# Optimization experiments

Hardware: AMD Instinct MI355X
Metric: run time of the kernel (lower is better)

The kernel has to match this reference:

```python
import jax, jax.numpy as jnp
import numpy as np

EPS = 1e-5  # BatchNorm2d default eps


def _bn(x, gamma, beta, mean, var):
    # inference-mode BN over channel dim (NCHW)
    inv = gamma / jnp.sqrt(var + EPS)
    return x * inv[None, :, None, None] + (beta - mean * inv)[None, :, None, None]


def _shift(x):
    # 4 channel groups shifted by 1 pixel in 4 directions, zero-fill at borders
    C = x.shape[1]
    gc = C // 4
    g0, g1, g2, g3 = (x[:, i * gc:(i + 1) * gc] for i in range(4))
    g0 = jnp.pad(g0[:, :, :, :-1], ((0, 0), (0, 0), (0, 0), (1, 0)))  # shift right (W)
    g1 = jnp.pad(g1[:, :, 1:, :], ((0, 0), (0, 0), (0, 1), (0, 0)))   # shift up (H)
    g2 = jnp.pad(g2[:, :, :, 1:], ((0, 0), (0, 0), (0, 0), (0, 1)))   # shift left (W)
    g3 = jnp.pad(g3[:, :, :-1, :], ((0, 0), (0, 0), (1, 0), (0, 0)))  # shift down (H)
    return jnp.concatenate([g0, g1, g2, g3], axis=1)


def setup_inputs() -> dict:
    key = jax.random.key(0)
    ks = jax.random.split(key, 8)
    B, C1, C2, H, W = 16, 128, 256, 128, 128
    x = jax.random.normal(ks[0], (B, C1, H, W), dtype=jnp.float32)
    w_conv = jax.random.normal(ks[1], (C2, C1, 3, 3), dtype=jnp.float32) * (1.0 / np.sqrt(C1 * 9))
    w_1x1 = jax.random.normal(ks[2], (C2, C2, 1, 1), dtype=jnp.float32) * (1.0 / np.sqrt(C2))
    b_1x1 = jax.random.normal(ks[3], (C2,), dtype=jnp.float32) * 0.05
    gamma = jax.random.uniform(ks[4], (C2,), dtype=jnp.float32, minval=0.5, maxval=1.5)
    beta = jax.random.normal(ks[5], (C2,), dtype=jnp.float32) * 0.1
    bn_mean = jax.random.normal(ks[6], (C2,), dtype=jnp.float32) * 0.1
    bn_var = jax.random.uniform(ks[7], (C2,), dtype=jnp.float32, minval=0.5, maxval=1.5)
    return {"x": x, "w_conv": w_conv, "w_1x1": w_1x1, "b_1x1": b_1x1,
            "gamma": gamma, "beta": beta, "bn_mean": bn_mean, "bn_var": bn_var}


def reference(x, w_conv, w_1x1, b_1x1, gamma, beta, bn_mean, bn_var):
    # conv3x3 (stride 1, 'same' via autopad=1, no bias) + BN + SiLU
    y = jax.lax.conv_general_dilated(
        x, w_conv, window_strides=(1, 1), padding=((1, 1), (1, 1)),
        dimension_numbers=("NCHW", "OIHW", "NCHW"))
    y = jax.nn.silu(_bn(y, gamma, beta, bn_mean, bn_var))
    identity = y
    # shift + conv1x1 (with bias) + same BN + residual + SiLU
    z = _shift(y)
    z = jax.lax.conv_general_dilated(
        z, w_1x1, window_strides=(1, 1), padding=((0, 0), (0, 0)),
        dimension_numbers=("NCHW", "OIHW", "NCHW")) + b_1x1[None, :, None, None]
    z = _bn(z, gamma, beta, bn_mean, bn_var) + identity
    return jax.nn.silu(z)
```

## Files before the change

kernel.cpp:

```cpp
#include <hip/hip_runtime.h>

typedef unsigned short u16;
typedef unsigned int   u32;
typedef __bf16 bf16x8 __attribute__((ext_vector_type(8)));
typedef float  f32x4  __attribute__((ext_vector_type(4)));

__device__ __forceinline__ float bf2f(u16 v){ u32 u = ((u32)v) << 16; float f; __builtin_memcpy(&f,&u,4); return f; }
__device__ __forceinline__ u16 f2bf(float f){ u32 u; __builtin_memcpy(&u,&f,4); u32 r = (u + 0x7FFFu + ((u>>16)&1u)) >> 16; return (u16)r; }
__device__ __forceinline__ float silu(float v){ return v / (1.f + __expf(-v)); }

__device__ __forceinline__ void gload_lds16(const u16* g, u16* l){
  __builtin_amdgcn_global_load_lds((const __attribute__((address_space(1))) void*)g,
                                   (__attribute__((address_space(3))) void*)l, 16, 0, 0);
}

#define FENCE asm volatile("" ::: "memory")
#define BARRIER do{ FENCE; __builtin_amdgcn_s_barrier(); FENCE; }while(0)

#define HP 130
#define XPIX 128
#define YPIX 256
#define XIMG (HP*HP*XPIX)
#define YIMG (HP*HP*YPIX)

__global__ void prep_coef(const float* __restrict__ gamma, const float* __restrict__ beta,
                          const float* __restrict__ mean,  const float* __restrict__ var,
                          const float* __restrict__ b1, float2* __restrict__ coefA, float2* __restrict__ coefB){
  int c = threadIdx.x;
  float s = gamma[c] * rsqrtf(var[c] + 1e-5f);
  float t = beta[c] - mean[c] * s;
  coefA[c] = make_float2(s, t);
  coefB[c] = make_float2(s, b1[c] * s + t);
}

__global__ void repack_w3(const float* __restrict__ w, u16* __restrict__ w3p){
  int idx = blockIdx.x*256 + threadIdx.x;
  int n = idx / 1152, k = idx % 1152;
  int tap = k >> 7, c = k & 127;
  int kh = tap / 3, kw = tap % 3;
  w3p[idx] = f2bf(w[((n*128 + c)*3 + kh)*3 + kw]);
}

__global__ void repack_w1(const float* __restrict__ w, u16* __restrict__ w1p){
  int idx = blockIdx.x*256 + threadIdx.x;
  w1p[idx] = f2bf(w[idx]);
}

__device__ __forceinline__ void halo_pix(int pi, int& hp, int& wp){
  if (pi < 130){ hp = 0; wp = pi; }
  else if (pi < 260){ hp = 129; wp = pi - 130; }
  else { int j = pi - 260; hp = 1 + (j >> 1); wp = (j & 1) ? 129 : 0; }
}
__global__ void zero_halos(u16* __restrict__ xpad, u16* __restrict__ ypad, int cimg){
  int idx = blockIdx.x*256 + threadIdx.x;
  const int NX = cimg*516*16;
  uint4 z = make_uint4(0u,0u,0u,0u);
  if (idx < NX){
    int b = idx / (516*16), rr = idx % (516*16);
    int pi = rr >> 4, cch = rr & 15, hp, wp;
    halo_pix(pi, hp, wp);
    *(uint4*)(xpad + (((size_t)b*HP + hp)*HP + wp)*XPIX + cch*8) = z;
  } else {
    idx -= NX;
    if (idx < cimg*516*32){
      int b = idx / (516*32), rr = idx % (516*32);
      int pi = rr >> 5, cch = rr & 31, hp, wp;
      halo_pix(pi, hp, wp);
      *(uint4*)(ypad + (((size_t)b*HP + hp)*HP + wp)*YPIX + cch*8) = z;
    }
  }
}

__global__ __launch_bounds__(256) void transpose_x(const float* __restrict__ x, u16* __restrict__ xpad, int b0){
  __shared__ u16 s[64][66];
  const int tid = threadIdx.x, bid = blockIdx.x;
  const int ct = bid & 1, wt = (bid >> 1) & 1, row = bid >> 2;
  const int bl = row >> 7, h = row & 127;
  const int c0 = ct << 6, w0 = wt << 6;
  {
    const int lw = tid & 63, lc4 = tid >> 6;
    const size_t xb = ((size_t)(b0 + bl)*128)*16384 + (size_t)h*128 + w0 + lw;
    #pragma unroll
    for (int r = 0; r < 16; ++r){
      int c = r*4 + lc4;
      s[c][lw] = f2bf(x[xb + (size_t)(c0 + c)*16384]);
    }
  }
  __syncthreads();
  {
    const int lw = tid >> 5, lcp = (tid & 31) << 1;
    const size_t pb = ((size_t)bl*HP + h + 1)*HP;
    #pragma unroll
    for (int r = 0; r < 8; ++r){
      int w = r*8 + lw;
      u32 v = (u32)s[lcp][w] | ((u32)s[lcp+1][w] << 16);
      *(u32*)(xpad + (pb + (w0 + w + 1))*XPIX + c0 + lcp) = v;
    }
  }
}


struct StgDesc { const u16* g[2][2]; int l[2][2]; };

__device__ __forceinline__ int offA_of(int Ts){
  int tap = Ts >> 1;
  int kh = (tap*11) >> 5;
  int kw = tap - kh*3;
  return kh*(HP*XPIX) + kw*XPIX + ((Ts & 1) << 6);
}

template<int V>
__device__ __forceinline__ void stage2(u16* lds, const StgDesc& d, int offE){
  gload_lds16(d.g[V][0] + offE, lds + d.l[V][0]);
  gload_lds16(d.g[V][1] + offE, lds + d.l[V][1]);
}

__global__ __launch_bounds__(512, 2) void convA(const u16* __restrict__ xpad, const u16* __restrict__ w3p,
                                                const float2* __restrict__ coefA, u16* __restrict__ ypad){
  __shared__ u16 sA[2][256*64];
  __shared__ u16 sB[2][256*64];
  const int t = threadIdx.x;
  const int nwg = gridDim.x;
  const int bid = blockIdx.x;
  const int bsz = (bid & 7)*(nwg >> 3) + (bid >> 3);
  const int bl = bsz >> 6;
  const int h0 = (bsz & 63) << 1;
  const int lane = t & 63, wave = t >> 6;
  const int wm = wave & 1, wn = wave >> 1;
  const int quad = lane >> 4, l16 = lane & 15;
  const int lc = t & 7;
  const u16* ximg = xpad + (size_t)bl * XIMG;

  StgDesc da, db;
  #pragma unroll
  for (int ho = 0; ho < 2; ++ho)
    #pragma unroll
    for (int q = 0; q < 2; ++q){
      int r = ((t >> 6) << 4) + (q << 3) + ((t >> 3) & 7);
      int p = (ho << 6) + r + (r & 64);
      da.g[ho][q] = ximg + (size_t)((h0 + (p >> 7))*HP + (p & 127))*XPIX + ((lc ^ (p & 7)) << 3);
      da.l[ho][q] = p*64 + lc*8;
    }
  #pragma unroll
  for (int bo = 0; bo < 2; ++bo)
    #pragma unroll
    for (int q = 0; q < 2; ++q){
      int r = ((t >> 6) << 4) + (q << 3) + ((t >> 3) & 7);
      int n = ((r >> 5) << 6) + (bo << 5) + (r & 31);
      db.g[bo][q] = w3p + (size_t)n*1152 + ((lc ^ (n & 7)) << 3);
      db.l[bo][q] = n*64 + lc*8;
    }

  u32 fA[4][2][2], fB[2][2][2];
  #pragma unroll
  for (int i = 0; i < 4; ++i)
    #pragma unroll
    for (int hf = 0; hf < 2; ++hf)
      #pragma unroll
      for (int c = 0; c < 2; ++c){
        int row = wm*128 + hf*64 + i*16 + l16;
        fA[i][hf][c] = row*64 + (((c*4 + quad) ^ (row & 7)) << 3);
      }
  #pragma unroll
  for (int j = 0; j < 2; ++j)
    #pragma unroll
    for (int hf = 0; hf < 2; ++hf)
      #pragma unroll
      for (int c = 0; c < 2; ++c){
        int row = wn*64 + hf*32 + j*16 + l16;
        fB[j][hf][c] = row*64 + (((c*4 + quad) ^ (row & 7)) << 3);
      }

  f32x4 acc[8][4];
  #pragma unroll
  for (int i = 0; i < 8; ++i)
    #pragma unroll
    for (int j = 0; j < 4; ++j){ f32x4 z = {0.f,0.f,0.f,0.f}; acc[i][j] = z; }

  {
    const int o0 = offA_of(0), o1 = offA_of(1);
    stage2<0>(sA[0], da, o0);
    stage2<0>(sB[0], db, 0);
    stage2<1>(sB[0], db, 0);
    stage2<1>(sA[0], da, o0);
    stage2<0>(sA[1], da, o1);
    stage2<0>(sB[1], db, 64);
    stage2<1>(sB[1], db, 64);
    asm volatile("s_waitcnt vmcnt(6)" ::: "memory");
  }
  BARRIER;

  for (int T = 0; T < 18; ++T){
    const int pr = T & 1;
    const u16* A = sA[pr];
    const u16* B = sB[pr];
    u16* An = sA[pr ^ 1];
    bf16x8 a[4][2], b0[2][2], b1[2][2];

    #pragma unroll
    for (int i = 0; i < 4; ++i){
      a[i][0] = *(const bf16x8*)(A + fA[i][0][0]);
      a[i][1] = *(const bf16x8*)(A + fA[i][0][1]);
    }
    #pragma unroll
    for (int j = 0; j < 2; ++j){
      b0[j][0] = *(const bf16x8*)(B + fB[j][0][0]);
      b0[j][1] = *(const bf16x8*)(B + fB[j][0][1]);
    }
    if (T + 1 < 18) stage2<1>(An, da, offA_of(T+1));
    BARRIER;
    __builtin_amdgcn_s_setprio(1);
    #pragma unroll
    for (int i = 0; i < 4; ++i)
      #pragma unroll
      for (int j = 0; j < 2; ++j){
        acc[i][j] = __builtin_amdgcn_mfma_f32_16x16x32_bf16(a[i][0], b0[j][0], acc[i][j], 0, 0, 0);
        acc[i][j] = __builtin_amdgcn_mfma_f32_16x16x32_bf16(a[i][1], b0[j][1], acc[i][j], 0, 0, 0);
      }
    __builtin_amdgcn_s_setprio(0);
    BARRIER;

    #pragma unroll
    for (int j = 0; j < 2; ++j){
      b1[j][0] = *(const bf16x8*)(B + fB[j][1][0]);
      b1[j][1] = *(const bf16x8*)(B + fB[j][1][1]);
    }
    if (T + 2 < 18) stage2<0>((u16*)A, da, offA_of(T+2));
    BARRIER;
    __builtin_amdgcn_s_setprio(1);
    #pragma unroll
    for (int i = 0; i < 4; ++i)
      #pragma unroll
      for (int j = 0; j < 2; ++j){
        acc[i][2+j] = __builtin_amdgcn_mfma_f32_16x16x32_bf16(a[i][0], b1[j][0], acc[i][2+j], 0, 0, 0);
        acc[i][2+j] = __builtin_amdgcn_mfma_f32_16x16x32_bf16(a[i][1], b1[j][1], acc[i][2+j], 0, 0, 0);
      }
    __builtin_amdgcn_s_setprio(0);
    BARRIER;

    #pragma unroll
    for (int i = 0; i < 4; ++i){
      a[i][0] = *(const bf16x8*)(A + fA[i][1][0]);
      a[i][1] = *(const bf16x8*)(A + fA[i][1][1]);
    }
    if (T + 2 < 18) stage2<0>((u16*)(B), db, (T+2)*64);
    BARRIER;
    __builtin_amdgcn_s_setprio(1);
    #pragma unroll
    for (int i = 0; i < 4; ++i)
      #pragma unroll
      for (int j = 0; j < 2; ++j){
        acc[4+i][2+j] = __builtin_amdgcn_mfma_f32_16x16x32_bf16(a[i][0], b1[j][0], acc[4+i][2+j], 0, 0, 0);
        acc[4+i][2+j] = __builtin_amdgcn_mfma_f32_16x16x32_bf16(a[i][1], b1[j][1], acc[4+i][2+j], 0, 0, 0);
      }
    __builtin_amdgcn_s_setprio(0);
    BARRIER;

    if (T + 2 < 18) stage2<1>((u16*)(B), db, (T+2)*64);
    BARRIER;
    __builtin_amdgcn_s_setprio(1);
    #pragma unroll
    for (int i = 0; i < 4; ++i)
      #pragma unroll
      for (int j = 0; j < 2; ++j){
        acc[4+i][j] = __builtin_amdgcn_mfma_f32_16x16x32_bf16(a[i][0], b0[j][0], acc[4+i][j], 0, 0, 0);
        acc[4+i][j] = __builtin_amdgcn_mfma_f32_16x16x32_bf16(a[i][1], b0[j][1], acc[4+i][j], 0, 0, 0);
      }
    __builtin_amdgcn_s_setprio(0);
    if (T < 16)       asm volatile("s_waitcnt vmcnt(6)" ::: "memory");
    else if (T == 16) asm volatile("s_waitcnt vmcnt(0)" ::: "memory");
    BARRIER;
  }

  float2 co[4];
  #pragma unroll
  for (int j = 0; j < 4; ++j) co[j] = coefA[wn*64 + j*16 + l16];
  #pragma unroll
  for (int ig = 0; ig < 8; ++ig){
    const int pb = wm*128 + ig*16 + quad*4;
    #pragma unroll
    for (int r = 0; r < 4; ++r){
      const int p = pb + r;
      const int hh = h0 + (p >> 7), ww = p & 127;
      u16* dst = ypad + ((size_t)(bl*HP + hh + 1)*HP + (ww + 1))*YPIX + wn*64;
      #pragma unroll
      for (int j = 0; j < 4; ++j){
        float v = acc[ig][j][r]*co[j].x + co[j].y;
        dst[j*16 + l16] = f2bf(silu(v));
      }
    }
  }
}

__device__ __forceinline__ void stgB(u16* act, u16* w, const u16* __restrict__ ypad,
                                     size_t imgy, int h, int kt, int r0, int sub, int tid,
                                     const u16* w_row0, const u16* w_row1){
  const int g = kt >> 1;
  const int dhp = (g == 0 || g == 2) ? 1 : (g == 1 ? 2 : 0);
  const int dwp = (g == 1 || g == 3) ? 1 : (g == 0 ? 0 : 2);
  const size_t rb = imgy + (size_t)((h + dhp)*HP)*YPIX + kt*32 + sub*8;
  gload_lds16(ypad + rb + (size_t)(r0 + dwp)*YPIX,      act + tid*8);
  gload_lds16(ypad + rb + (size_t)(r0 + 64 + dwp)*YPIX, act + 2048 + tid*8);
  gload_lds16(w_row0 + kt*32, w + tid*8);
  gload_lds16(w_row1 + kt*32, w + 2048 + tid*8);
}

__global__ __launch_bounds__(256) void convB(const u16* __restrict__ ypad, const u16* __restrict__ w1p,
                                             const float2* __restrict__ coefB, float* __restrict__ out, int b0){
  __shared__ u16 sAct[2][4096];
  __shared__ u16 sW[2][4096];
  const int tid = threadIdx.x;
  const int nwg = gridDim.x;
  const int bidl = (blockIdx.x & 7)*(nwg >> 3) + (blockIdx.x >> 3);
  const int nt = bidl & 1, row = bidl >> 1;
  const int bl = row >> 7, h = row & 127;
  const int n0 = nt << 7;
  const int lane = tid & 63, wave = tid >> 6;
  const int wc = wave & 1, wpx = wave >> 1;
  const int quad = lane >> 4, l16 = lane & 15;
  const int r0 = tid >> 2, sub = tid & 3;

  f32x4 acc[4][4];
  #pragma unroll
  for (int i = 0; i < 4; ++i)
    #pragma unroll
    for (int j = 0; j < 4; ++j){ f32x4 zz = {0.f,0.f,0.f,0.f}; acc[i][j] = zz; }

  const size_t imgy = (size_t)bl * YIMG;
  const u16* w_row0 = w1p + (size_t)(n0 + r0)*256 + sub*8;
  const u16* w_row1 = w_row0 + (size_t)64*256;

  stgB(sAct[0], sW[0], ypad, imgy, h, 0, r0, sub, tid, w_row0, w_row1);
  asm volatile("s_waitcnt vmcnt(0)" ::: "memory");
  BARRIER;

  #pragma unroll
  for (int kt = 0; kt < 8; ++kt){
    const int cur = kt & 1;
    if (kt < 7) stgB(sAct[cur^1], sW[cur^1], ypad, imgy, h, kt+1, r0, sub, tid, w_row0, w_row1);

    bf16x8 wf[4], af[4];
    #pragma unroll
    for (int i = 0; i < 4; ++i) wf[i] = *(const bf16x8*)&sW[cur][(wc*64 + i*16 + l16)*32 + quad*8];
    #pragma unroll
    for (int j = 0; j < 4; ++j) af[j] = *(const bf16x8*)&sAct[cur][(wpx*64 + j*16 + l16)*32 + quad*8];
    __builtin_amdgcn_s_setprio(1);
    #pragma unroll
    for (int i = 0; i < 4; ++i)
      #pragma unroll
      for (int j = 0; j < 4; ++j)
        acc[i][j] = __builtin_amdgcn_mfma_f32_16x16x32_bf16(wf[i], af[j], acc[i][j], 0, 0, 0);
    __builtin_amdgcn_s_setprio(0);
    asm volatile("s_waitcnt vmcnt(0)" ::: "memory");
    BARRIER;
  }

  const size_t ybase = ((size_t)(bl*HP + h + 1))*HP*YPIX;
  const size_t obase = (size_t)(b0 + bl)*256*16384 + (size_t)h*128;
  #pragma unroll
  for (int i = 0; i < 4; ++i){
    const int chb = n0 + wc*64 + i*16 + quad*4;
    const float2 c0 = coefB[chb+0], c1 = coefB[chb+1], c2 = coefB[chb+2], c3 = coefB[chb+3];
    float* ob = out + obase + (size_t)chb*16384;
    #pragma unroll
    for (int j = 0; j < 4; ++j){
      const int p = wpx*64 + j*16 + l16;
      const ushort4 rv = *(const ushort4*)&ypad[ybase + (size_t)(p + 1)*YPIX + chb];
      ob[p]             = silu(acc[i][j][0]*c0.x + c0.y + bf2f(rv.x));
      ob[16384 + p]     = silu(acc[i][j][1]*c1.x + c1.y + bf2f(rv.y));
      ob[2*16384 + p]   = silu(acc[i][j][2]*c2.x + c2.y + bf2f(rv.z));
      ob[3*16384 + p]   = silu(acc[i][j][3]*c3.x + c3.y + bf2f(rv.w));
    }
  }
}

extern "C" void kernel_launch(void* const* d_in, const int* in_sizes, int n_in,
                              void* d_out, int out_size, void* d_ws, size_t ws_size,
                              hipStream_t stream){
  const float* x  = (const float*)d_in[0];
  const float* w3 = (const float*)d_in[1];
  const float* w1 = (const float*)d_in[2];
  const float* b1 = (const float*)d_in[3];
  const float* gm = (const float*)d_in[4];
  const float* bt = (const float*)d_in[5];
  const float* mn = (const float*)d_in[6];
  const float* vr = (const float*)d_in[7];
  float* outp = (float*)d_out;

  char* ws = (char*)d_ws;
  float2* coefA = (float2*)ws;
  float2* coefB = coefA + 256;
  u16*    w3p   = (u16*)(ws + 4096);
  u16*    w1p   = (u16*)(ws + 4096 + 589824);
  const size_t fixed = 4096 + 589824 + 131072;
  int cimg = 16;
  while (cimg > 1 && fixed + (size_t)cimg*12979200ull > ws_size) cimg >>= 1;
  u16* xpad = (u16*)(ws + fixed);
  u16* ypad = (u16*)(ws + fixed + (size_t)cimg*4326400ull);

  prep_coef<<<1, 256, 0, stream>>>(gm, bt, mn, vr, b1, coefA, coefB);
  repack_w3<<<1152, 256, 0, stream>>>(w3, w3p);
  repack_w1<<<256, 256, 0, stream>>>(w1, w1p);
  {
    int nthr = cimg*516*48;
    zero_halos<<<(nthr + 255)/256, 256, 0, stream>>>(xpad, ypad, cimg);
  }
  for (int b0 = 0; b0 < 16; b0 += cimg){
    transpose_x<<<4*128*cimg, 256, 0, stream>>>(x, xpad, b0);
    convA<<<64*cimg, 512, 0, stream>>>(xpad, w3p, coefA, ypad);
    convB<<<2*128*cimg, 256, 0, stream>>>(ypad, w1p, coefB, outp, b0);
  }
}
```

Measured before the change: 668.5 us.

## Make convA persistent over multiple row bands with a simplified two-phase pipeline; widen convB K-tile

convA now handles BPW consecutive 2-row bands per workgroup (grid shrunk accordingly) with a continuous double-buffered loop that prefetches the next band's first tile while finishing the current one. The per-K-step schedule is cut from four MFMA phases with barriers to two, loading all B fragments at once, and the epilogue runs inline between bands. convB moves to 64-channel K-tiles with XOR-swizzled LDS, so there are 4 stages instead of 8, and declares 2 blocks per SM. These aim to reduce launch and prologue overhead, barrier count and LDS bank conflicts, at the cost of higher register pressure and fewer, longer-lived workgroups (possible tail imbalance).

```diff
diff --git a/kernel.cpp b/kernel.cpp
--- a/kernel.cpp
+++ b/kernel.cpp
@@ -100,8 +100,6 @@
 }
 
 
-struct StgDesc { const u16* g[2][2]; int l[2][2]; };
-
 __device__ __forceinline__ int offA_of(int Ts){
   int tap = Ts >> 1;
   int kh = (tap*11) >> 5;
@@ -109,67 +107,55 @@
   return kh*(HP*XPIX) + kw*XPIX + ((Ts & 1) << 6);
 }
 
-template<int V>
-__device__ __forceinline__ void stage2(u16* lds, const StgDesc& d, int offE){
-  gload_lds16(d.g[V][0] + offE, lds + d.l[V][0]);
-  gload_lds16(d.g[V][1] + offE, lds + d.l[V][1]);
-}
-
 __global__ __launch_bounds__(512, 2) void convA(const u16* __restrict__ xpad, const u16* __restrict__ w3p,
-                                                const float2* __restrict__ coefA, u16* __restrict__ ypad){
-  __shared__ u16 sA[2][256*64];
-  __shared__ u16 sB[2][256*64];
+                                                const float2* __restrict__ coefA, u16* __restrict__ ypad,
+                                                int BPW){
+  __shared__ u16 sA[2][16384];
+  __shared__ u16 sB[2][16384];
   const int t = threadIdx.x;
   const int nwg = gridDim.x;
-  const int bid = blockIdx.x;
-  const int bsz = (bid & 7)*(nwg >> 3) + (bid >> 3);
-  const int bl = bsz >> 6;
-  const int h0 = (bsz & 63) << 1;
+  const int w = (blockIdx.x & 7)*(nwg >> 3) + (blockIdx.x >> 3);
+  const int band0 = w * BPW;
+  const int bl = band0 >> 6;
+  int h0 = (band0 & 63) << 1;
   const int lane = t & 63, wave = t >> 6;
   const int wm = wave & 1, wn = wave >> 1;
   const int quad = lane >> 4, l16 = lane & 15;
   const int lc = t & 7;
   const u16* ximg = xpad + (size_t)bl * XIMG;
 
-  StgDesc da, db;
+  const u16* gA[2][2]; int lA[2][2];
+  const u16* gB[2][2]; int lB[2][2];
   #pragma unroll
   for (int ho = 0; ho < 2; ++ho)
     #pragma unroll
     for (int q = 0; q < 2; ++q){
       int r = ((t >> 6) << 4) + (q << 3) + ((t >> 3) & 7);
       int p = (ho << 6) + r + (r & 64);
-      da.g[ho][q] = ximg + (size_t)((h0 + (p >> 7))*HP + (p & 127))*XPIX + ((lc ^ (p & 7)) << 3);
-      da.l[ho][q] = p*64 + lc*8;
-    }
-  #pragma unroll
-  for (int bo = 0; bo < 2; ++bo)
-    #pragma unroll
-    for (int q = 0; q < 2; ++q){
-      int r = ((t >> 6) << 4) + (q << 3) + ((t >> 3) & 7);
-      int n = ((r >> 5) << 6) + (bo << 5) + (r & 31);
-      db.g[bo][q] = w3p + (size_t)n*1152 + ((lc ^ (n & 7)) << 3);
-      db.l[bo][q] = n*64 + lc*8;
-    }
-
-  u32 fA[4][2][2], fB[2][2][2];
-  #pragma unroll
-  for (int i = 0; i < 4; ++i)
-    #pragma unroll
-    for (int hf = 0; hf < 2; ++hf)
+      gA[ho][q] = ximg + (size_t)((h0 + (p >> 7))*HP + (p & 127))*XPIX + ((lc ^ (p & 7)) << 3);
+      lA[ho][q] = p*64 + lc*8;
+      int n = ((r >> 5) << 6) + (ho << 5) + (r & 31);
+      gB[ho][q] = w3p + (size_t)n*1152 + ((lc ^ (n & 7)) << 3);
+      lB[ho][q] = n*64 + lc*8;
+    }
+
+  u32 fA[2][4][2], fB[4][2];
+  #pragma unroll
+  for (int hf = 0; hf < 2; ++hf)
+    #pragma unroll
+    for (int i = 0; i < 4; ++i)
       #pragma unroll
       for (int c = 0; c < 2; ++c){
         int row = wm*128 + hf*64 + i*16 + l16;
-        fA[i][hf][c] = row*64 + (((c*4 + quad) ^ (row & 7)) << 3);
-      }
-  #pragma unroll
-  for (int j = 0; j < 2; ++j)
-    #pragma unroll
-    for (int hf = 0; hf < 2; ++hf)
-      #pragma unroll
-      for (int c = 0; c < 2; ++c){
-        int row = wn*64 + hf*32 + j*16 + l16;
-        fB[j][hf][c] = row*64 + (((c*4 + quad) ^ (row & 7)) << 3);
-      }
+        fA[hf][i][c] = row*64 + (((c*4 + quad) ^ (row & 7)) << 3);
+      }
+  #pragma unroll
+  for (int j = 0; j < 4; ++j)
+    #pragma unroll
+    for (int c = 0; c < 2; ++c){
+      int row = wn*64 + j*16 + l16;
+      fB[j][c] = row*64 + (((c*4 + quad) ^ (row & 7)) << 3);
+    }
 
   f32x4 acc[8][4];
   #pragma unroll
@@ -178,137 +164,113 @@
     for (int j = 0; j < 4; ++j){ f32x4 z = {0.f,0.f,0.f,0.f}; acc[i][j] = z; }
 
   {
-    const int o0 = offA_of(0), o1 = offA_of(1);
-    stage2<0>(sA[0], da, o0);
-    stage2<0>(sB[0], db, 0);
-    stage2<1>(sB[0], db, 0);
-    stage2<1>(sA[0], da, o0);
-    stage2<0>(sA[1], da, o1);
-    stage2<0>(sB[1], db, 64);
-    stage2<1>(sB[1], db, 64);
-    asm volatile("s_waitcnt vmcnt(6)" ::: "memory");
+    gload_lds16(gA[0][0], sA[0] + lA[0][0]); gload_lds16(gA[0][1], sA[0] + lA[0][1]);
+    gload_lds16(gB[0][0], sB[0] + lB[0][0]); gload_lds16(gB[0][1], sB[0] + lB[0][1]);
+    gload_lds16(gB[1][0], sB[0] + lB[1][0]); gload_lds16(gB[1][1], sB[0] + lB[1][1]);
+    gload_lds16(gA[1][0], sA[0] + lA[1][0]); gload_lds16(gA[1][1], sA[0] + lA[1][1]);
+    asm volatile("s_waitcnt vmcnt(0)" ::: "memory");
   }
   BARRIER;
 
-  for (int T = 0; T < 18; ++T){
-    const int pr = T & 1;
-    const u16* A = sA[pr];
-    const u16* B = sB[pr];
-    u16* An = sA[pr ^ 1];
-    bf16x8 a[4][2], b0[2][2], b1[2][2];
-
+  const int UTOT = 18 * BPW;
+  int tn = 0;
+  for (int u = 0; u < UTOT; ++u){
+    const int pr = u & 1;
+    const u16* A = sA[pr]; const u16* B = sB[pr];
+    u16* An = sA[pr ^ 1]; u16* Bn = sB[pr ^ 1];
+    const bool last = (u == UTOT - 1);
+    const int ntl = (tn == 17) ? 0 : tn + 1;
+    if (tn == 17 && !last){
+      #pragma unroll
+      for (int ho = 0; ho < 2; ++ho)
+        #pragma unroll
+        for (int q = 0; q < 2; ++q) gA[ho][q] += 2*HP*XPIX;
+    }
+    const int aoff = offA_of(ntl), boff = ntl*64;
+
+    bf16x8 a[4][2], b[4][2];
     #pragma unroll
     for (int i = 0; i < 4; ++i){
-      a[i][0] = *(const bf16x8*)(A + fA[i][0][0]);
-      a[i][1] = *(const bf16x8*)(A + fA[i][0][1]);
-    }
-    #pragma unroll
-    for (int j = 0; j < 2; ++j){
-      b0[j][0] = *(const bf16x8*)(B + fB[j][0][0]);
-      b0[j][1] = *(const bf16x8*)(B + fB[j][0][1]);
-    }
-    if (T + 1 < 18) stage2<1>(An, da, offA_of(T+1));
+      a[i][0] = *(const bf16x8*)(A + fA[0][i][0]);
+      a[i][1] = *(const bf16x8*)(A + fA[0][i][1]);
+    }
+    #pragma unroll
+    for (int j = 0; j < 4; ++j){
+      b[j][0] = *(const bf16x8*)(B + fB[j][0]);
+      b[j][1] = *(const bf16x8*)(B + fB[j][1]);
+    }
+    if (!last){
+      gload_lds16(gA[0][0] + aoff, An + lA[0][0]); gload_lds16(gA[0][1] + aoff, An + lA[0][1]);
+      gload_lds16(gB[0][0] + boff, Bn + lB[0][0]); gload_lds16(gB[0][1] + boff, Bn + lB[0][1]);
+    }
+    __builtin_amdgcn_s_setprio(1);
+    #pragma unroll
+    for (int i = 0; i < 4; ++i)
+      #pragma unroll
+      for (int j = 0; j < 4; ++j){
+        acc[i][j] = __builtin_amdgcn_mfma_f32_16x16x32_bf16(a[i][0], b[j][0], acc[i][j], 0, 0, 0);
+        acc[i][j] = __builtin_amdgcn_mfma_f32_16x16x32_bf16(a[i][1], b[j][1], acc[i][j], 0, 0, 0);
+      }
+    __builtin_amdgcn_s_setprio(0);
+    if (last) asm volatile("s_waitcnt vmcnt(0)" ::: "memory");
+    else      asm volatile("s_waitcnt vmcnt(4)" ::: "memory");
     BARRIER;
+
+    #pragma unroll
+    for (int i = 0; i < 4; ++i){
+      a[i][0] = *(const bf16x8*)(A + fA[1][i][0]);
+      a[i][1] = *(const bf16x8*)(A + fA[1][i][1]);
+    }
+    if (!last){
+      gload_lds16(gB[1][0] + boff, Bn + lB[1][0]); gload_lds16(gB[1][1] + boff, Bn + lB[1][1]);
+      gload_lds16(gA[1][0] + aoff, An + lA[1][0]); gload_lds16(gA[1][1] + aoff, An + lA[1][1]);
+    }
     __builtin_amdgcn_s_setprio(1);
     #pragma unroll
     for (int i = 0; i < 4; ++i)
       #pragma unroll
-      for (int j = 0; j < 2; ++j){
-        acc[i][j] = __builtin_amdgcn_mfma_f32_16x16x32_bf16(a[i][0], b0[j][0], acc[i][j], 0, 0, 0);
-        acc[i][j] = __builtin_amdgcn_mfma_f32_16x16x32_bf16(a[i][1], b0[j][1], acc[i][j], 0, 0, 0);
+      for (int j = 0; j < 4; ++j){
+        acc[4+i][j] = __builtin_amdgcn_mfma_f32_16x16x32_bf16(a[i][0], b[j][0], acc[4+i][j], 0, 0, 0);
+        acc[4+i][j] = __builtin_amdgcn_mfma_f32_16x16x32_bf16(a[i][1], b[j][1], acc[4+i][j], 0, 0, 0);
       }
     __builtin_amdgcn_s_setprio(0);
+    if (!last) asm volatile("s_waitcnt vmcnt(2)" ::: "memory");
     BARRIER;
 
-    #pragma unroll
-    for (int j = 0; j < 2; ++j){
-      b1[j][0] = *(const bf16x8*)(B + fB[j][1][0]);
-      b1[j][1] = *(const bf16x8*)(B + fB[j][1][1]);
-    }
-    if (T + 2 < 18) stage2<0>((u16*)A, da, offA_of(T+2));
-    BARRIER;
-    __builtin_amdgcn_s_setprio(1);
-    #pragma unroll
-    for (int i = 0; i < 4; ++i)
-      #pragma unroll
-      for (int j = 0; j < 2; ++j){
-        acc[i][2+j] = __builtin_amdgcn_mfma_f32_16x16x32_bf16(a[i][0], b1[j][0], acc[i][2+j], 0, 0, 0);
-        acc[i][2+j] = __builtin_amdgcn_mfma_f32_16x16x32_bf16(a[i][1], b1[j][1], acc[i][2+j], 0, 0, 0);
-      }
-    __builtin_amdgcn_s_setprio(0);
-    BARRIER;
-
-    #pragma unroll
-    for (int i = 0; i < 4; ++i){
-      a[i][0] = *(const bf16x8*)(A + fA[i][1][0]);
-      a[i][1] = *(const bf16x8*)(A + fA[i][1][1]);
-    }
-    if (T + 2 < 18) stage2<0>((u16*)(B), db, (T+2)*64);
-    BARRIER;
-    __builtin_amdgcn_s_setprio(1);
-    #pragma unroll
-    for (int i = 0; i < 4; ++i)
-      #pragma unroll
-      for (int j = 0; j < 2; ++j){
-        acc[4+i][2+j] = __builtin_amdgcn_mfma_f32_16x16x32_bf16(a[i][0], b1[j][0], acc[4+i][2+j], 0, 0, 0);
-        acc[4+i][2+j] = __builtin_amdgcn_mfma_f32_16x16x32_bf16(a[i][1], b1[j][1], acc[4+i][2+j], 0, 0, 0);
-      }
-    __builtin_amdgcn_s_setprio(0);
-    BARRIER;
-
-    if (T + 2 < 18) stage2<1>((u16*)(B), db, (T+2)*64);
-    BARRIER;
-    __builtin_amdgcn_s_setprio(1);
-    #pragma unroll
-    for (int i = 0; i < 4; ++i)
-      #pragma unroll
-      for (int j = 0; j < 2; ++j){
-        acc[4+i][j] = __builtin_amdgcn_mfma_f32_16x16x32_bf16(a[i][0], b0[j][0], acc[4+i][j], 0, 0, 0);
-        acc[4+i][j] = __builtin_amdgcn_mfma_f32_16x16x32_bf16(a[i][1], b0[j][1], acc[4+i][j], 0, 0, 0);
-      }
-    __builtin_amdgcn_s_setprio(0);
-    if (T < 16)       asm volatile("s_waitcnt vmcnt(6)" ::: "memory");
-    else if (T == 16) asm volatile("s_waitcnt vmcnt(0)" ::: "memory");
-    BARRIER;
-  }
-
-  float2 co[4];
-  #pragma unroll
-  for (int j = 0; j < 4; ++j) co[j] = coefA[wn*64 + j*16 + l16];
-  #pragma unroll
-  for (int ig = 0; ig < 8; ++ig){
-    const int pb = wm*128 + ig*16 + quad*4;
-    #pragma unroll
-    for (int r = 0; r < 4; ++r){
-      const int p = pb + r;
-      const int hh = h0 + (p >> 7), ww = p & 127;
-      u16* dst = ypad + ((size_t)(bl*HP + hh + 1)*HP + (ww + 1))*YPIX + wn*64;
-      #pragma unroll
-      for (int j = 0; j < 4; ++j){
-        float v = acc[ig][j][r]*co[j].x + co[j].y;
-        dst[j*16 + l16] = f2bf(silu(v));
-      }
-    }
-  }
-}
-
-__device__ __forceinline__ void stgB(u16* act, u16* w, const u16* __restrict__ ypad,
-                                     size_t imgy, int h, int kt, int r0, int sub, int tid,
-                                     const u16* w_row0, const u16* w_row1){
-  const int g = kt >> 1;
-  const int dhp = (g == 0 || g == 2) ? 1 : (g == 1 ? 2 : 0);
-  const int dwp = (g == 1 || g == 3) ? 1 : (g == 0 ? 0 : 2);
-  const size_t rb = imgy + (size_t)((h + dhp)*HP)*YPIX + kt*32 + sub*8;
-  gload_lds16(ypad + rb + (size_t)(r0 + dwp)*YPIX,      act + tid*8);
-  gload_lds16(ypad + rb + (size_t)(r0 + 64 + dwp)*YPIX, act + 2048 + tid*8);
-  gload_lds16(w_row0 + kt*32, w + tid*8);
-  gload_lds16(w_row1 + kt*32, w + 2048 + tid*8);
-}
-
-__global__ __launch_bounds__(256) void convB(const u16* __restrict__ ypad, const u16* __restrict__ w1p,
-                                             const float2* __restrict__ coefB, float* __restrict__ out, int b0){
-  __shared__ u16 sAct[2][4096];
-  __shared__ u16 sW[2][4096];
+    if (tn == 17){
+      float2 co[4];
+      #pragma unroll
+      for (int j = 0; j < 4; ++j) co[j] = coefA[wn*64 + j*16 + l16];
+      #pragma unroll
+      for (int ig = 0; ig < 8; ++ig){
+        const int pb = wm*128 + ig*16 + quad*4;
+        #pragma unroll
+        for (int r = 0; r < 4; ++r){
+          const int p = pb + r;
+          const int hh = h0 + (p >> 7), ww = p & 127;
+          u16* dst = ypad + ((size_t)(bl*HP + hh + 1)*HP + (ww + 1))*YPIX + wn*64;
+          #pragma unroll
+          for (int j = 0; j < 4; ++j){
+            float v = acc[ig][j][r]*co[j].x + co[j].y;
+            dst[j*16 + l16] = f2bf(silu(v));
+          }
+        }
+      }
+      asm volatile("s_waitcnt vmcnt(0)" ::: "memory");
+      h0 += 2;
+      tn = 0;
+      #pragma unroll
+      for (int i = 0; i < 8; ++i)
+        #pragma unroll
+        for (int j = 0; j < 4; ++j){ f32x4 z = {0.f,0.f,0.f,0.f}; acc[i][j] = z; }
+    } else ++tn;
+  }
+}
+
+__global__ __launch_bounds__(256, 2) void convB(const u16* __restrict__ ypad, const u16* __restrict__ w1p,
+                                                const float2* __restrict__ coefB, float* __restrict__ out, int b0){
+  __shared__ u16 sAct[2][8192];
+  __shared__ u16 sW[2][8192];
   const int tid = threadIdx.x;
   const int nwg = gridDim.x;
   const int bidl = (blockIdx.x & 7)*(nwg >> 3) + (blockIdx.x >> 3);
@@ -318,7 +280,29 @@
   const int lane = tid & 63, wave = tid >> 6;
   const int wc = wave & 1, wpx = wave >> 1;
   const int quad = lane >> 4, l16 = lane & 15;
-  const int r0 = tid >> 2, sub = tid & 3;
+
+  const size_t imgy = (size_t)bl * YIMG;
+
+  const u16* gact[4]; const u16* gwt[4]; int ldst[4];
+  #pragma unroll
+  for (int l = 0; l < 4; ++l){
+    int id = l*256 + tid;
+    int p = id >> 3, c = id & 7;
+    gact[l] = ypad + imgy + (size_t)(h*HP)*YPIX + (size_t)p*YPIX + ((c ^ (p & 7)) << 3);
+    gwt[l]  = w1p + (size_t)(n0 + p)*256 + ((c ^ (p & 7)) << 3);
+    ldst[l] = id*8;
+  }
+
+  u32 fW[4][2], fAc[4][2];
+  #pragma unroll
+  for (int i = 0; i < 4; ++i)
+    #pragma unroll
+    for (int k = 0; k < 2; ++k){
+      int rn = wc*64 + i*16 + l16;
+      fW[i][k] = rn*64 + (((k*4 + quad) ^ (rn & 7)) << 3);
+      int rp = wpx*64 + i*16 + l16;
+      fAc[i][k] = rp*64 + (((k*4 + quad) ^ (rp & 7)) << 3);
+    }
 
   f32x4 acc[4][4];
   #pragma unroll
@@ -326,30 +310,48 @@
     #pragma unroll
     for (int j = 0; j < 4; ++j){ f32x4 zz = {0.f,0.f,0.f,0.f}; acc[i][j] = zz; }
 
-  const size_t imgy = (size_t)bl * YIMG;
-  const u16* w_row0 = w1p + (size_t)(n0 + r0)*256 + sub*8;
-  const u16* w_row1 = w_row0 + (size_t)64*256;
-
-  stgB(sAct[0], sW[0], ypad, imgy, h, 0, r0, sub, tid, w_row0, w_row1);
-  asm volatile("s_waitcnt vmcnt(0)" ::: "memory");
+  {
+    const int aoff = (1*HP + 0)*YPIX + 0;
+    #pragma unroll
+    for (int l = 0; l < 4; ++l){
+      gload_lds16(gact[l] + aoff, sAct[0] + ldst[l]);
+      gload_lds16(gwt[l],         sW[0]   + ldst[l]);
+    }
+    asm volatile("s_waitcnt vmcnt(0)" ::: "memory");
+  }
   BARRIER;
 
   #pragma unroll
-  for (int kt = 0; kt < 8; ++kt){
-    const int cur = kt & 1;
-    if (kt < 7) stgB(sAct[cur^1], sW[cur^1], ypad, imgy, h, kt+1, r0, sub, tid, w_row0, w_row1);
-
-    bf16x8 wf[4], af[4];
-    #pragma unroll
-    for (int i = 0; i < 4; ++i) wf[i] = *(const bf16x8*)&sW[cur][(wc*64 + i*16 + l16)*32 + quad*8];
-    #pragma unroll
-    for (int j = 0; j < 4; ++j) af[j] = *(const bf16x8*)&sAct[cur][(wpx*64 + j*16 + l16)*32 + quad*8];
+  for (int g = 0; g < 4; ++g){
+    const int pr = g & 1;
+    if (g < 3){
+      const int gg = g + 1;
+      const int dhp = (gg == 1) ? 2 : ((gg == 3) ? 0 : 1);
+      const int dwp = (gg == 0) ? 0 : ((gg == 2) ? 2 : 1);
+      const int aoff = (dhp*HP + dwp)*YPIX + gg*64;
+      const int woff = gg*64;
+      #pragma unroll
+      for (int l = 0; l < 4; ++l){
+        gload_lds16(gact[l] + aoff, sAct[pr^1] + ldst[l]);
+        gload_lds16(gwt[l] + woff,  sW[pr^1]   + ldst[l]);
+      }
+    }
+    bf16x8 wf[4][2], af[4][2];
+    #pragma unroll
+    for (int i = 0; i < 4; ++i){
+      wf[i][0] = *(const bf16x8*)(sW[pr] + fW[i][0]);
+      wf[i][1] = *(const bf16x8*)(sW[pr] + fW[i][1]);
+      af[i][0] = *(const bf16x8*)(sAct[pr] + fAc[i][0]);
+      af[i][1] = *(const bf16x8*)(sAct[pr] + fAc[i][1]);
+    }
     __builtin_amdgcn_s_setprio(1);
     #pragma unroll
     for (int i = 0; i < 4; ++i)
       #pragma unroll
-      for (int j = 0; j < 4; ++j)
-        acc[i][j] = __builtin_amdgcn_mfma_f32_16x16x32_bf16(wf[i], af[j], acc[i][j], 0, 0, 0);
+      for (int j = 0; j < 4; ++j){
+        acc[i][j] = __builtin_amdgcn_mfma_f32_16x16x32_bf16(wf[i][0], af[j][0], acc[i][j], 0, 0, 0);
+        acc[i][j] = __builtin_amdgcn_mfma_f32_16x16x32_bf16(wf[i][1], af[j][1], acc[i][j], 0, 0, 0);
+      }
     __builtin_amdgcn_s_setprio(0);
     asm volatile("s_waitcnt vmcnt(0)" ::: "memory");
     BARRIER;
@@ -405,9 +407,12 @@
     int nthr = cimg*516*48;
     zero_halos<<<(nthr + 255)/256, 256, 0, stream>>>(xpad, ypad, cimg);
   }
+  const int bands = 64*cimg;
+  const int BPW = (bands >= 1024) ? 4 : (bands >= 512 ? 2 : 1);
+  const int nwgA = bands / BPW;
   for (int b0 = 0; b0 < 16; b0 += cimg){
     transpose_x<<<4*128*cimg, 256, 0, stream>>>(x, xpad, b0);
-    convA<<<64*cimg, 512, 0, stream>>>(xpad, w3p, coefA, ypad);
+    convA<<<nwgA, 512, 0, stream>>>(xpad, w3p, coefA, ypad, BPW);
     convB<<<2*128*cimg, 256, 0, stream>>>(ypad, w1p, coefB, outp, b0);
   }
 }
```

After: 651.0 us. 2.6% less time.
